# Optimization experiments

Measured on AMD Instinct MI355X. Metric: run time of the kernel, lower is better.

The kernel has to match this reference:

```python
import jax, jax.numpy as jnp
import numpy as np
from jax import lax

N_NODES = 32768   # 256 graphs x 128 nodes
N_GRAPHS = 256
DEG = 16          # fixed neighbor-list length per node
IN = 128
HID = 256
OUT = 16


def setup_inputs() -> dict:
    key = jax.random.key(0)
    ks = jax.random.split(key, 12)
    g = lambda k, s: jax.random.normal(k, s, dtype=jnp.float32) * 0.05
    return {
        "x": jax.random.normal(ks[0], (N_NODES, IN), dtype=jnp.float32),
        "neighbors": jax.random.randint(ks[1], (N_NODES, DEG), 0, N_NODES, dtype=jnp.int32),
        # conv1: LSTM(in=128, hid=128), fc_self/fc_neigh 128->256
        "Wi1": g(ks[2], (4 * IN, IN)),
        "Wh1": g(ks[3], (4 * IN, IN)),
        "bi1": jnp.zeros((4 * IN,), jnp.float32),
        "bh1": jnp.zeros((4 * IN,), jnp.float32),
        "Ws1": g(ks[4], (HID, IN)),
        "Wn1": g(ks[5], (HID, IN)),
        "b1": jnp.zeros((HID,), jnp.float32),
        # conv2: LSTM(in=256, hid=256), fc_self/fc_neigh 256->256
        "Wi2": g(ks[6], (4 * HID, HID)),
        "Wh2": g(ks[7], (4 * HID, HID)),
        "bi2": jnp.zeros((4 * HID,), jnp.float32),
        "bh2": jnp.zeros((4 * HID,), jnp.float32),
        "Ws2": g(ks[8], (HID, HID)),
        "Wn2": g(ks[9], (HID, HID)),
        "b2": jnp.zeros((HID,), jnp.float32),
        # classifier 256 -> 16
        "Wc": g(ks[10], (OUT, HID)),
        "bc": jnp.zeros((OUT,), jnp.float32),
    }


def _lstm_agg(h, neighbors, Wi, Wh, bi, bh):
    # DGL SAGEConv 'lstm' reducer: LSTM over each node's neighbor feature
    # sequence, hidden size == feature size; returns final hidden state.
    # h: [N, F], neighbors: [N, D]
    N, F = h.shape

    def step(carry, nbr_t):
        hs, cs = carry
        x = h[nbr_t]                                  # [N, F] gather
        gates = x @ Wi.T + hs @ Wh.T + (bi + bh)      # [N, 4F]
        i, f, g, o = jnp.split(gates, 4, axis=-1)     # PyTorch gate order
        c = jax.nn.sigmoid(f) * cs + jax.nn.sigmoid(i) * jnp.tanh(g)
        hn = jax.nn.sigmoid(o) * jnp.tanh(c)
        return (hn, c), None

    z = jnp.zeros((N, F), h.dtype)
    (hT, _), _ = lax.scan(step, (z, z), neighbors.T)  # scan over DEG steps
    return hT


def _sage_conv(h, neighbors, Wi, Wh, bi, bh, Ws, Wn, b):
    h_neigh = _lstm_agg(h, neighbors, Wi, Wh, bi, bh)
    return h @ Ws.T + h_neigh @ Wn.T + b


def reference(x, neighbors, Wi1, Wh1, bi1, bh1, Ws1, Wn1, b1,
              Wi2, Wh2, bi2, bh2, Ws2, Wn2, b2, Wc, bc):
    h = _sage_conv(x, neighbors, Wi1, Wh1, bi1, bh1, Ws1, Wn1, b1)
    h = jax.nn.relu(h)
    h = _sage_conv(h, neighbors, Wi2, Wh2, bi2, bh2, Ws2, Wn2, b2)
    h = jax.nn.relu(h)
    # dgl.mean_nodes over a batch of equal-size graphs
    hg = h.reshape(N_GRAPHS, N_NODES // N_GRAPHS, HID).mean(axis=1)  # [B, HID]
    return hg @ Wc.T + bc                                            # [B, OUT]
```

## Files before the change

kernel.cpp:

```cpp
#include <hip/hip_runtime.h>

#define N_NODES 32768
#define DEG 16
#define IN_F 128
#define HIDF 256
#define N_GRAPHS 256
#define NPG 128
#define OUT_F 16

typedef unsigned short u16;
typedef unsigned int u32;
typedef __bf16 bf16x8 __attribute__((ext_vector_type(8)));
typedef float f32x4 __attribute__((ext_vector_type(4)));
typedef u16 u16x4 __attribute__((ext_vector_type(4)));
typedef u16 u16x8 __attribute__((ext_vector_type(8)));

__device__ __forceinline__ u16 f2bf(float f) {
  union { float f; unsigned u; } v; v.f = f;
  return (u16)((v.u + 0x7FFFu + ((v.u >> 16) & 1u)) >> 16);
}
__device__ __forceinline__ float bf2f(u16 b) {
  union { unsigned u; float f; } v; v.u = ((unsigned)b) << 16;
  return v.f;
}
__device__ __forceinline__ float sigm(float x) { return 1.0f / (1.0f + __expf(-x)); }
__device__ __forceinline__ float tanhfast(float x) {
  float e = __expf(2.0f * x);
  return (e - 1.0f) / (e + 1.0f);
}


__global__ void k_prep_x(const float* __restrict__ x, u16* __restrict__ out, int n4) {
  int i = blockIdx.x * blockDim.x + threadIdx.x;
  if (i < n4) {
    float4 v = ((const float4*)x)[i];
    ushort4 o;
    o.x = f2bf(v.x); o.y = f2bf(v.y); o.z = f2bf(v.z); o.w = f2bf(v.w);
    ((ushort4*)out)[i] = o;
  }
}

__global__ void k_prep_wg(const float* __restrict__ Wi, const float* __restrict__ Wh,
                          const float* __restrict__ bi, const float* __restrict__ bh,
                          u16* __restrict__ Wip, u16* __restrict__ Whp,
                          float* __restrict__ bwp, int F) {
  int total = 4 * F * F;
  for (int idx = blockIdx.x * blockDim.x + threadIdx.x; idx < total;
       idx += gridDim.x * blockDim.x) {
    int p = idx / F, k = idx % F;
    {
      int fe = p >> 2, g = p & 3;
      int orig = g * F + fe;
      Whp[idx] = f2bf(Wh[orig * F + k]);
    }
    {
      int base = p & ~63, local = p & 63;
      int lq = local >> 4, mt = (local >> 2) & 3, gate = local & 3;
      int oldp = base + mt * 16 + lq * 4 + gate;
      int fe = oldp >> 2, g = oldp & 3;
      int orig = g * F + fe;
      Wip[idx] = f2bf(Wi[orig * F + k]);
      if (k == 0) bwp[p] = bi[orig] + bh[orig];
    }
  }
}

__global__ void k_prep_cast(const float* __restrict__ Ws, const float* __restrict__ Wn,
                            u16* __restrict__ Bs, u16* __restrict__ Bn, int n) {
  int i = blockIdx.x * blockDim.x + threadIdx.x;
  if (i < n) { Bs[i] = f2bf(Ws[i]); Bn[i] = f2bf(Wn[i]); }
}

template <int K, int NC>
__launch_bounds__(256, 4)
__global__ void k_gemm(const u16* __restrict__ A, const u16* __restrict__ B,
                       const float* __restrict__ bias, u16* __restrict__ C) {
  constexpr int ROWB = 2 * K;
  __shared__ u16 lds[64 * K];
  char* ldsb = (char*)lds;
  const int tid = threadIdx.x;
  const int w = tid >> 6;
  const int lane = tid & 63;
  const int l16 = lane & 15, lq = lane >> 4;
  const int row0 = blockIdx.x * 64;
  const int col0 = blockIdx.y * 128;

  constexpr int CH = K / 8;
  constexpr int RPI = 256 / CH;
#pragma unroll
  for (int it = 0; it < 64 / RPI; ++it) {
    int r = tid / CH + it * RPI;
    int ch = tid % CH;
    bf16x8 v = *(const bf16x8*)(A + (size_t)(row0 + r) * K + ch * 8);
    int bo = r * ROWB + ((ch * 16) ^ ((r & 7) << 4));
    *(bf16x8*)(ldsb + bo) = v;
  }
  __syncthreads();

  f32x4 acc[4][2];
#pragma unroll
  for (int mt = 0; mt < 4; ++mt)
#pragma unroll
    for (int nt = 0; nt < 2; ++nt)
#pragma unroll
      for (int j = 0; j < 4; ++j) acc[mt][nt][j] = 0.f;

  for (int ks = 0; ks < K / 32; ++ks) {
    bf16x8 a[4];
#pragma unroll
    for (int mt = 0; mt < 4; ++mt) {
      int r = mt * 16 + l16;
      int bo = r * ROWB + (((ks * 32 + lq * 8) * 2) ^ ((r & 7) << 4));
      a[mt] = *(const bf16x8*)(ldsb + bo);
    }
#pragma unroll
    for (int nt = 0; nt < 2; ++nt) {
      int coln = col0 + w * 32 + nt * 16 + l16;
      bf16x8 b = *(const bf16x8*)(B + (size_t)coln * K + ks * 32 + lq * 8);
#pragma unroll
      for (int mt = 0; mt < 4; ++mt)
        acc[mt][nt] = __builtin_amdgcn_mfma_f32_16x16x32_bf16(a[mt], b, acc[mt][nt], 0, 0, 0);
    }
  }
#pragma unroll
  for (int mt = 0; mt < 4; ++mt)
#pragma unroll
    for (int nt = 0; nt < 2; ++nt) {
      int coln = col0 + w * 32 + nt * 16 + l16;
      float bb = bias[coln];
#pragma unroll
      for (int j = 0; j < 4; ++j) {
        int r = row0 + mt * 16 + lq * 4 + j;
        C[(size_t)r * NC + coln] = f2bf(acc[mt][nt][j] + bb);
      }
    }
}

template <int K>
__launch_bounds__(256, 4)
__global__ void k_comb(const u16* __restrict__ A, const u16* __restrict__ B,
                       const u16* __restrict__ XS, u16* __restrict__ C) {
  constexpr int ROWB = 2 * K;
  __shared__ u16 lds[64 * K];
  char* ldsb = (char*)lds;
  const int tid = threadIdx.x;
  const int w = tid >> 6;
  const int lane = tid & 63;
  const int l16 = lane & 15, lq = lane >> 4;
  const int row0 = blockIdx.x * 64;
  const int col0 = blockIdx.y * 128;

  constexpr int CH = K / 8;
  constexpr int RPI = 256 / CH;
#pragma unroll
  for (int it = 0; it < 64 / RPI; ++it) {
    int r = tid / CH + it * RPI;
    int ch = tid % CH;
    bf16x8 v = *(const bf16x8*)(A + (size_t)(row0 + r) * K + ch * 8);
    int bo = r * ROWB + ((ch * 16) ^ ((r & 7) << 4));
    *(bf16x8*)(ldsb + bo) = v;
  }
  __syncthreads();

  f32x4 acc[4][2];
#pragma unroll
  for (int mt = 0; mt < 4; ++mt)
#pragma unroll
    for (int nt = 0; nt < 2; ++nt)
#pragma unroll
      for (int j = 0; j < 4; ++j) acc[mt][nt][j] = 0.f;

  for (int ks = 0; ks < K / 32; ++ks) {
    bf16x8 a[4];
#pragma unroll
    for (int mt = 0; mt < 4; ++mt) {
      int r = mt * 16 + l16;
      int bo = r * ROWB + (((ks * 32 + lq * 8) * 2) ^ ((r & 7) << 4));
      a[mt] = *(const bf16x8*)(ldsb + bo);
    }
#pragma unroll
    for (int nt = 0; nt < 2; ++nt) {
      int coln = col0 + w * 32 + nt * 16 + l16;
      bf16x8 b = *(const bf16x8*)(B + (size_t)coln * K + ks * 32 + lq * 8);
#pragma unroll
      for (int mt = 0; mt < 4; ++mt)
        acc[mt][nt] = __builtin_amdgcn_mfma_f32_16x16x32_bf16(a[mt], b, acc[mt][nt], 0, 0, 0);
    }
  }
#pragma unroll
  for (int mt = 0; mt < 4; ++mt)
#pragma unroll
    for (int nt = 0; nt < 2; ++nt) {
      int coln = col0 + w * 32 + nt * 16 + l16;
#pragma unroll
      for (int j = 0; j < 4; ++j) {
        int r = row0 + mt * 16 + lq * 4 + j;
        float v = acc[mt][nt][j] + bf2f(XS[(size_t)r * HIDF + coln]);
        C[(size_t)r * HIDF + coln] = f2bf(fmaxf(v, 0.f));
      }
    }
}

template <int F, bool T0>
__launch_bounds__(512, 4)
__global__ void k_step(const u16* __restrict__ hprev,
                       const u16* __restrict__ XW,
                       const u16* __restrict__ Whp,
                       const int* __restrict__ nbr,
                       int t,
                       u16* __restrict__ cT,
                       u16* __restrict__ hnext) {
  constexpr int ROWB = 2 * F;
  constexpr int KS = F / 32;
  constexpr int RBN = F / 16;
  __shared__ __align__(16) u16 Alds[64 * F];
  __shared__ __align__(16) u16 tl[256 * 24];
  char* ldsb = (char*)Alds;
  const int tid = threadIdx.x;
  const int w = tid >> 6;
  const int lane = tid & 63;
  const int l16 = lane & 15, lq = lane >> 4;

  const int p = blockIdx.x + RBN * blockIdx.y;
  const int s = p >> 3;
  const int rb = s % RBN;
  const int g = (p & 7) + 8 * (s / RBN);

  const int row0 = rb * 64;
  const int col0 = g * 256;
  const int feb = row0 >> 2;
  const int n0 = col0 + w * 32 + l16;
  const int n1 = n0 + 16;

  const int nb0 = nbr[(size_t)n0 * DEG + t];
  const int nb1 = nbr[(size_t)n1 * DEG + t];

  if constexpr (!T0) {
    constexpr int CH = F / 8;
    constexpr int RPI = 512 / CH;
#pragma unroll
    for (int it = 0; it < 64 / RPI; ++it) {
      int r = tid / CH + it * RPI;
      int ch = tid % CH;
      bf16x8 v = *(const bf16x8*)(Whp + (size_t)(row0 + r) * F + ch * 8);
      int bo = r * ROWB + ((ch * 16) ^ ((r & 7) << 4));
      *(bf16x8*)(ldsb + bo) = v;
    }
  }

  u16x8 xwv[2][2];
  {
    const u16* b0 = XW + (size_t)nb0 * (4 * F) + row0 + lq * 16;
    const u16* b1 = XW + (size_t)nb1 * (4 * F) + row0 + lq * 16;
    xwv[0][0] = *(const u16x8*)(b0);
    xwv[0][1] = *(const u16x8*)(b0 + 8);
    xwv[1][0] = *(const u16x8*)(b1);
    xwv[1][1] = *(const u16x8*)(b1 + 8);
  }

  float cold[4][2];
  if constexpr (!T0) {
#pragma unroll
    for (int mt = 0; mt < 4; ++mt) {
      cold[mt][0] = bf2f(cT[(size_t)(feb + mt * 4 + lq) * N_NODES + n0]);
      cold[mt][1] = bf2f(cT[(size_t)(feb + mt * 4 + lq) * N_NODES + n1]);
    }
  }

  f32x4 acc[4][2];
#pragma unroll
  for (int mt = 0; mt < 4; ++mt)
#pragma unroll
    for (int nt = 0; nt < 2; ++nt)
#pragma unroll
      for (int j = 0; j < 4; ++j) acc[mt][nt][j] = 0.f;

  if constexpr (!T0) {
    __syncthreads();
    const u16* hb0 = hprev + (size_t)n0 * F + lq * 8;
    const u16* hb1 = hprev + (size_t)n1 * F + lq * 8;
#pragma unroll
    for (int ks = 0; ks < KS; ++ks) {
      bf16x8 b0 = *(const bf16x8*)(hb0 + ks * 32);
      bf16x8 b1 = *(const bf16x8*)(hb1 + ks * 32);
      bf16x8 a[4];
#pragma unroll
      for (int mt = 0; mt < 4; ++mt) {
        int r = mt * 16 + l16;
        int bo = r * ROWB + (((ks * 32 + lq * 8) * 2) ^ ((r & 7) << 4));
        a[mt] = *(const bf16x8*)(ldsb + bo);
      }
#pragma unroll
      for (int mt = 0; mt < 4; ++mt) {
        acc[mt][0] = __builtin_amdgcn_mfma_f32_16x16x32_bf16(a[mt], b0, acc[mt][0], 0, 0, 0);
        acc[mt][1] = __builtin_amdgcn_mfma_f32_16x16x32_bf16(a[mt], b1, acc[mt][1], 0, 0, 0);
      }
    }
  }

#pragma unroll
  for (int mt = 0; mt < 4; ++mt) {
    int fe = feb + mt * 4 + lq;
#pragma unroll
    for (int nt = 0; nt < 2; ++nt) {
      int n = nt ? n1 : n0;
      float pi, pf, pg, po;
      if (mt < 2) {
        pi = acc[mt][nt][0] + bf2f(xwv[nt][0][(mt & 1) * 4 + 0]);
        pf = acc[mt][nt][1] + bf2f(xwv[nt][0][(mt & 1) * 4 + 1]);
        pg = acc[mt][nt][2] + bf2f(xwv[nt][0][(mt & 1) * 4 + 2]);
        po = acc[mt][nt][3] + bf2f(xwv[nt][0][(mt & 1) * 4 + 3]);
      } else {
        pi = acc[mt][nt][0] + bf2f(xwv[nt][1][(mt & 1) * 4 + 0]);
        pf = acc[mt][nt][1] + bf2f(xwv[nt][1][(mt & 1) * 4 + 1]);
        pg = acc[mt][nt][2] + bf2f(xwv[nt][1][(mt & 1) * 4 + 2]);
        po = acc[mt][nt][3] + bf2f(xwv[nt][1][(mt & 1) * 4 + 3]);
      }
      float cn;
      if constexpr (T0) cn = sigm(pi) * tanhfast(pg);
      else              cn = sigm(pf) * cold[mt][nt] + sigm(pi) * tanhfast(pg);
      float hn = sigm(po) * tanhfast(cn);
      cT[(size_t)fe * N_NODES + n] = f2bf(cn);
      tl[(w * 32 + nt * 16 + l16) * 24 + mt * 4 + lq] = f2bf(hn);
    }
  }
  __syncthreads();
  {
    int nloc = tid >> 1, q = tid & 1;
    u16x8 v = *(const u16x8*)&tl[nloc * 24 + q * 8];
    *(u16x8*)(hnext + (size_t)(col0 + nloc) * F + feb + q * 8) = v;
  }
}

__global__ void k_pool(const u16* __restrict__ h2, const float* __restrict__ Wc,
                       const float* __restrict__ bc, float* __restrict__ out) {
  __shared__ float hg[HIDF];
  int g = blockIdx.x;
  int tid = threadIdx.x;
  float s = 0.0f;
  for (int i = 0; i < NPG; ++i) s += bf2f(h2[(size_t)(g * NPG + i) * HIDF + tid]);
  hg[tid] = s * (1.0f / NPG);
  __syncthreads();
  if (tid < OUT_F) {
    float o = bc[tid];
    for (int fe = 0; fe < HIDF; ++fe) o += hg[fe] * Wc[tid * HIDF + fe];
    out[g * OUT_F + tid] = o;
  }
}

extern "C" void kernel_launch(void* const* d_in, const int* in_sizes, int n_in,
                              void* d_out, int out_size, void* d_ws, size_t ws_size,
                              hipStream_t stream) {
  const float* x   = (const float*)d_in[0];
  const int*   nbr = (const int*)d_in[1];
  const float* Wi1 = (const float*)d_in[2];
  const float* Wh1 = (const float*)d_in[3];
  const float* bi1 = (const float*)d_in[4];
  const float* bh1 = (const float*)d_in[5];
  const float* Ws1 = (const float*)d_in[6];
  const float* Wn1 = (const float*)d_in[7];
  const float* b1  = (const float*)d_in[8];
  const float* Wi2 = (const float*)d_in[9];
  const float* Wh2 = (const float*)d_in[10];
  const float* bi2 = (const float*)d_in[11];
  const float* bh2 = (const float*)d_in[12];
  const float* Ws2 = (const float*)d_in[13];
  const float* Wn2 = (const float*)d_in[14];
  const float* b2  = (const float*)d_in[15];
  const float* Wc  = (const float*)d_in[16];
  const float* bc  = (const float*)d_in[17];
  float* out = (float*)d_out;

  char* ws = (char*)d_ws;
  const size_t MB = 1u << 20;
  u16*   x16 = (u16*)(ws + 0);
  u16*   XW1 = (u16*)(ws + 8 * MB);
  u16*   XS1 = (u16*)(ws + 40 * MB);
  u16*   X2  = XS1;
  u16*   hA1 = (u16*)(ws + 56 * MB);
  u16*   hB1 = (u16*)(ws + 64 * MB);
  u16*   c1  = (u16*)(ws + 72 * MB);
  u16*   XW2 = (u16*)(ws + 80 * MB);
  u16*   XS2 = (u16*)(ws + 0);
  u16*   h2o = XS2;
  u16*   hA2 = (u16*)(ws + 16 * MB);
  u16*   hB2 = (u16*)(ws + 32 * MB);
  u16*   c2  = (u16*)(ws + 56 * MB);
  char* wr = ws + 144 * MB;
  size_t off = 0;
  auto alloc = [&](size_t bytes) { void* p = wr + off; off += (bytes + 255) & ~(size_t)255; return p; };
  u16*   Wip1 = (u16*)alloc(512 * 128 * 2);
  u16*   Whp1 = (u16*)alloc(512 * 128 * 2);
  float* bwp1 = (float*)alloc(512 * 4);
  u16*   Bs1  = (u16*)alloc(256 * 128 * 2);
  u16*   Bn1  = (u16*)alloc(256 * 128 * 2);
  u16*   Wip2 = (u16*)alloc(1024 * 256 * 2);
  u16*   Whp2 = (u16*)alloc(1024 * 256 * 2);
  float* bwp2 = (float*)alloc(1024 * 4);
  u16*   Bs2  = (u16*)alloc(256 * 256 * 2);
  u16*   Bn2  = (u16*)alloc(256 * 256 * 2);

  k_prep_x<<<dim3(N_NODES * IN_F / 4 / 256), dim3(256), 0, stream>>>(x, x16, N_NODES * IN_F / 4);
  k_prep_wg<<<dim3(256), dim3(256), 0, stream>>>(Wi1, Wh1, bi1, bh1, Wip1, Whp1, bwp1, IN_F);
  k_prep_wg<<<dim3(1024), dim3(256), 0, stream>>>(Wi2, Wh2, bi2, bh2, Wip2, Whp2, bwp2, HIDF);
  k_prep_cast<<<dim3(128), dim3(256), 0, stream>>>(Ws1, Wn1, Bs1, Bn1, 256 * 128);
  k_prep_cast<<<dim3(256), dim3(256), 0, stream>>>(Ws2, Wn2, Bs2, Bn2, 256 * 256);

  k_gemm<128, 512><<<dim3(N_NODES / 64, 4), dim3(256), 0, stream>>>(x16, Wip1, bwp1, XW1);
  k_gemm<128, 256><<<dim3(N_NODES / 64, 2), dim3(256), 0, stream>>>(x16, Bs1, b1, XS1);
  {
    k_step<IN_F, true><<<dim3(8, N_NODES / 256), dim3(512), 0, stream>>>(
        hA1, XW1, Whp1, nbr, 0, c1, hA1);
    u16* hc = hA1; u16* hn = hB1;
    for (int t = 1; t < DEG; ++t) {
      k_step<IN_F, false><<<dim3(8, N_NODES / 256), dim3(512), 0, stream>>>(
          hc, XW1, Whp1, nbr, t, c1, hn);
      u16* tmp = hc; hc = hn; hn = tmp;
    }
    k_comb<128><<<dim3(N_NODES / 64, 2), dim3(256), 0, stream>>>(hc, Bn1, XS1, X2);
  }

  k_gemm<256, 1024><<<dim3(N_NODES / 64, 8), dim3(256), 0, stream>>>(X2, Wip2, bwp2, XW2);
  k_gemm<256, 256><<<dim3(N_NODES / 64, 2), dim3(256), 0, stream>>>(X2, Bs2, b2, XS2);
  {
    k_step<HIDF, true><<<dim3(16, N_NODES / 256), dim3(512), 0, stream>>>(
        hA2, XW2, Whp2, nbr, 0, c2, hA2);
    u16* hc = hA2; u16* hn = hB2;
    for (int t = 1; t < DEG; ++t) {
      k_step<HIDF, false><<<dim3(16, N_NODES / 256), dim3(512), 0, stream>>>(
          hc, XW2, Whp2, nbr, t, c2, hn);
      u16* tmp = hc; hc = hn; hn = tmp;
    }
    k_comb<256><<<dim3(N_NODES / 64, 2), dim3(256), 0, stream>>>(hc, Bn2, XS2, h2o);
  }

  k_pool<<<dim3(N_GRAPHS), dim3(256), 0, stream>>>(h2o, Wc, bc, out);
}
```

Baseline: 1.284 ms.

## Fuse layer-1 LSTM time steps into a single persistent kernel

Measured after the change: 1.161 ms. -9.6%, faster.

```diff
diff --git a/kernel.cpp b/kernel.cpp
--- a/kernel.cpp
+++ b/kernel.cpp
@@ -199,6 +199,129 @@
         C[(size_t)r * HIDF + coln] = f2bf(fmaxf(v, 0.f));
       }
     }
+}
+
+template <int F>
+__launch_bounds__(512, 2)
+__global__ void k_layer(const u16* __restrict__ XW,
+                        const u16* __restrict__ Whp,
+                        const int* __restrict__ nbr,
+                        u16* __restrict__ hout) {
+  constexpr int NT = 64;
+  constexpr int KS = F / 32;
+  constexpr int ROWB = 2 * F;
+  __shared__ __align__(16) u16 Wst[8 * 64 * F];
+  __shared__ __align__(16) u16 hbuf[NT * F];
+  __shared__ int snbrT[DEG * NT];
+  const int tid = threadIdx.x;
+  const int w = tid >> 6;
+  const int lane = tid & 63;
+  const int l16 = lane & 15, lq = lane >> 4;
+  const int nodeg = blockIdx.x * NT;
+  const int row0 = w * 64;
+
+#pragma unroll
+  for (int it = 0; it < 16; ++it) {
+    int idx = it * 512 + tid;
+    int r = idx >> 4;
+    int ch = idx & 15;
+    bf16x8 v = *(const bf16x8*)(Whp + (size_t)r * F + ch * 8);
+    int s = r >> 6, rr = r & 63;
+    char* base = (char*)Wst + (size_t)s * (64 * ROWB);
+    int bo = rr * ROWB + ((ch * 16) ^ ((rr & 7) << 4));
+    *(bf16x8*)(base + bo) = v;
+  }
+  for (int idx = tid; idx < DEG * NT; idx += 512) {
+    int nl = idx / DEG, tt = idx % DEG;
+    snbrT[tt * NT + nl] = nbr[(size_t)(nodeg + nl) * DEG + tt];
+  }
+
+  float c[4][4];
+#pragma unroll
+  for (int mt = 0; mt < 4; ++mt)
+#pragma unroll
+    for (int nt = 0; nt < 4; ++nt) c[mt][nt] = 0.f;
+
+  __syncthreads();
+
+  const char* wb = (const char*)Wst + (size_t)w * (64 * ROWB);
+  const char* hb = (const char*)hbuf;
+  char* hw = (char*)hbuf;
+
+#pragma unroll 1
+  for (int t = 0; t < DEG; ++t) {
+    u16x8 xwv[4][2];
+#pragma unroll
+    for (int nt = 0; nt < 4; ++nt) {
+      int nb = snbrT[t * NT + nt * 16 + l16];
+      const u16* bp = XW + (size_t)nb * (4 * F) + row0 + lq * 16;
+      xwv[nt][0] = *(const u16x8*)(bp);
+      xwv[nt][1] = *(const u16x8*)(bp + 8);
+    }
+
+    f32x4 acc[4][4];
+#pragma unroll
+    for (int mt = 0; mt < 4; ++mt)
+#pragma unroll
+      for (int nt = 0; nt < 4; ++nt)
+#pragma unroll
+        for (int j = 0; j < 4; ++j) acc[mt][nt][j] = 0.f;
+
+    __syncthreads();
+    if (t > 0) {
+#pragma unroll
+      for (int ks = 0; ks < KS; ++ks) {
+        bf16x8 a[4];
+#pragma unroll
+        for (int mt = 0; mt < 4; ++mt) {
+          int rr = mt * 16 + l16;
+          int bo = rr * ROWB + (((ks * 32 + lq * 8) * 2) ^ ((rr & 7) << 4));
+          a[mt] = *(const bf16x8*)(wb + bo);
+        }
+        bf16x8 b[4];
+#pragma unroll
+        for (int nt = 0; nt < 4; ++nt) {
+          int nl = nt * 16 + l16;
+          int bo = nl * ROWB + (((ks * 32 + lq * 8) * 2) ^ ((nl & 7) << 4));
+          b[nt] = *(const bf16x8*)(hb + bo);
+        }
+#pragma unroll
+        for (int mt = 0; mt < 4; ++mt)
+#pragma unroll
+          for (int nt = 0; nt < 4; ++nt)
+            acc[mt][nt] = __builtin_amdgcn_mfma_f32_16x16x32_bf16(a[mt], b[nt], acc[mt][nt], 0, 0, 0);
+      }
+    }
+    __syncthreads();
+
+#pragma unroll
+    for (int mt = 0; mt < 4; ++mt) {
+      int fe = w * 16 + mt * 4 + lq;
+      const int h2 = mt >> 1, q4 = (mt & 1) * 4;
+#pragma unroll
+      for (int nt = 0; nt < 4; ++nt) {
+        int nl = nt * 16 + l16;
+        float pi = acc[mt][nt][0] + bf2f(xwv[nt][h2][q4 + 0]);
+        float pf = acc[mt][nt][1] + bf2f(xwv[nt][h2][q4 + 1]);
+        float pg = acc[mt][nt][2] + bf2f(xwv[nt][h2][q4 + 2]);
+        float po = acc[mt][nt][3] + bf2f(xwv[nt][h2][q4 + 3]);
+        float cn = sigm(pf) * c[mt][nt] + sigm(pi) * tanhfast(pg);
+        c[mt][nt] = cn;
+        float hn = sigm(po) * tanhfast(cn);
+        int bo = nl * ROWB + ((fe * 2) ^ ((nl & 7) << 4));
+        *(u16*)(hw + bo) = f2bf(hn);
+      }
+    }
+  }
+  __syncthreads();
+
+  constexpr int CPN = F / 8;
+  for (int idx = tid; idx < NT * CPN; idx += 512) {
+    int nl = idx / CPN, fg = idx % CPN;
+    int bo = nl * ROWB + ((fg * 16) ^ ((nl & 7) << 4));
+    u16x8 v = *(const u16x8*)(hb + bo);
+    *(u16x8*)(hout + (size_t)(nodeg + nl) * F + fg * 8) = v;
+  }
 }
 
 template <int F, bool T0>
@@ -378,8 +501,6 @@
   u16*   XS1 = (u16*)(ws + 40 * MB);
   u16*   X2  = XS1;
   u16*   hA1 = (u16*)(ws + 56 * MB);
-  u16*   hB1 = (u16*)(ws + 64 * MB);
-  u16*   c1  = (u16*)(ws + 72 * MB);
   u16*   XW2 = (u16*)(ws + 80 * MB);
   u16*   XS2 = (u16*)(ws + 0);
   u16*   h2o = XS2;
@@ -408,17 +529,8 @@
 
   k_gemm<128, 512><<<dim3(N_NODES / 64, 4), dim3(256), 0, stream>>>(x16, Wip1, bwp1, XW1);
   k_gemm<128, 256><<<dim3(N_NODES / 64, 2), dim3(256), 0, stream>>>(x16, Bs1, b1, XS1);
-  {
-    k_step<IN_F, true><<<dim3(8, N_NODES / 256), dim3(512), 0, stream>>>(
-        hA1, XW1, Whp1, nbr, 0, c1, hA1);
-    u16* hc = hA1; u16* hn = hB1;
-    for (int t = 1; t < DEG; ++t) {
-      k_step<IN_F, false><<<dim3(8, N_NODES / 256), dim3(512), 0, stream>>>(
-          hc, XW1, Whp1, nbr, t, c1, hn);
-      u16* tmp = hc; hc = hn; hn = tmp;
-    }
-    k_comb<128><<<dim3(N_NODES / 64, 2), dim3(256), 0, stream>>>(hc, Bn1, XS1, X2);
-  }
+  k_layer<IN_F><<<dim3(N_NODES / 64), dim3(512), 0, stream>>>(XW1, Whp1, nbr, hA1);
+  k_comb<128><<<dim3(N_NODES / 64, 2), dim3(256), 0, stream>>>(hA1, Bn1, XS1, X2);
 
   k_gemm<256, 1024><<<dim3(N_NODES / 64, 8), dim3(256), 0, stream>>>(X2, Wip2, bwp2, XW2);
   k_gemm<256, 256><<<dim3(N_NODES / 64, 2), dim3(256), 0, stream>>>(X2, Bs2, b2, XS2);
```
